# Optimization experiments

Measured on AMD Instinct MI355X. Metric: run time of the kernel, lower is better.

The kernel has to match this reference:

```python
import jax, jax.numpy as jnp
import numpy as np
from jax import lax

B, T, F = 64, 2048, 40
CF, K = 8, 3              # conv filters, kernel size
Ho, Wo = T - K + 1, F - K + 1   # valid conv output: (2046, 38)
GIN, GH, ATT = Wo * CF, 32, 32  # GRU input 304, hidden 32, attn 32


def setup_inputs() -> dict:
    key = jax.random.key(0)
    ks = jax.random.split(key, 16)
    s = 0.1
    return {
        "x": jax.random.normal(ks[0], (B, 1, T, F), jnp.float32),
        "offset_w": jax.random.normal(ks[1], (2 * K * K, 1, K, K), jnp.float32) * s,
        "offset_b": jnp.zeros((2 * K * K,), jnp.float32),
        "dcn_w": jax.random.normal(ks[2], (CF, 1, K, K), jnp.float32) * s,
        "dcn_b": jax.random.normal(ks[3], (CF,), jnp.float32) * s,
        "w_ih": jax.random.normal(ks[4], (3 * GH, GIN), jnp.float32) * s,
        "w_hh": jax.random.normal(ks[5], (3 * GH, GH), jnp.float32) * s,
        "b_ih": jax.random.normal(ks[6], (3 * GH,), jnp.float32) * s,
        "b_hh": jax.random.normal(ks[7], (3 * GH,), jnp.float32) * s,
        "w1": jax.random.normal(ks[8], (ATT, GH), jnp.float32) * s,
        "b1": jax.random.normal(ks[9], (ATT,), jnp.float32) * s,
        "w2": jax.random.normal(ks[10], (GH, ATT), jnp.float32) * s,
        "b2": jax.random.normal(ks[11], (GH,), jnp.float32) * s,
        "w3": jax.random.normal(ks[12], (2, GH), jnp.float32) * s,
        "b3": jax.random.normal(ks[13], (2,), jnp.float32) * s,
    }


def _bilinear(img, ph, pw):
    # img: (H, W); ph, pw: (Ho, Wo, K*K) float sampling coords
    H, W = img.shape
    ph = jnp.clip(ph, 0.0, H - 1.0)
    pw = jnp.clip(pw, 0.0, W - 1.0)
    h0 = jnp.floor(ph).astype(jnp.int32)
    w0 = jnp.floor(pw).astype(jnp.int32)
    h1 = jnp.minimum(h0 + 1, H - 1)
    w1 = jnp.minimum(w0 + 1, W - 1)
    lh = ph - h0.astype(ph.dtype)
    lw = pw - w0.astype(pw.dtype)
    v00 = img[h0, w0]
    v01 = img[h0, w1]
    v10 = img[h1, w0]
    v11 = img[h1, w1]
    return (v00 * (1 - lh) * (1 - lw) + v01 * (1 - lh) * lw
            + v10 * lh * (1 - lw) + v11 * lh * lw)


def _deform_conv(x, offset_w, offset_b, dcn_w, dcn_b):
    # offset conv (valid): (B, 2*K*K, Ho, Wo)
    offset = lax.conv_general_dilated(
        x, offset_w, (1, 1), 'VALID',
        dimension_numbers=('NCHW', 'OIHW', 'NCHW')) + offset_b[None, :, None, None]
    off_h = offset[:, :K * K].transpose(0, 2, 3, 1)   # (B, Ho, Wo, 9)
    off_w = offset[:, K * K:].transpose(0, 2, 3, 1)
    ki = jnp.repeat(jnp.arange(K, dtype=x.dtype), K)  # kernel row index per tap
    kj = jnp.tile(jnp.arange(K, dtype=x.dtype), K)    # kernel col index per tap
    base_h = (jnp.arange(Ho, dtype=x.dtype)[:, None] + ki)[:, None, :]  # (Ho,1,9)
    base_w = (jnp.arange(Wo, dtype=x.dtype)[:, None] + kj)[None, :, :]  # (1,Wo,9)
    ph = off_h + base_h   # (B, Ho, Wo, 9)
    pw = off_w + base_w
    samp = jax.vmap(_bilinear)(x[:, 0], ph, pw)       # (B, Ho, Wo, 9)
    out = jnp.einsum('bhwk,ok->bohw', samp, dcn_w.reshape(CF, K * K))
    out = out + dcn_b[None, :, None, None]            # (B, CF, Ho, Wo)
    return out, offset


def _gru(xs, w_ih, w_hh, b_ih, b_hh):
    # xs: (T, B, GIN); PyTorch GRU gate order r, z, n
    gi_all = jnp.einsum('tbi,gi->tbg', xs, w_ih) + b_ih  # precompute input gates
    h0 = jnp.zeros((xs.shape[1], GH), xs.dtype)

    def step(h, gi):
        gh = h @ w_hh.T + b_hh
        ir, iz, inn = jnp.split(gi, 3, axis=-1)
        hr, hz, hn = jnp.split(gh, 3, axis=-1)
        r = jax.nn.sigmoid(ir + hr)
        z = jax.nn.sigmoid(iz + hz)
        n = jnp.tanh(inn + r * hn)
        h = (1 - z) * n + z * h
        return h, h

    _, ys = lax.scan(step, h0, gi_all)
    return ys  # (T, B, GH)


def reference(x, offset_w, offset_b, dcn_w, dcn_b,
              w_ih, w_hh, b_ih, b_hh, w1, b1, w2, b2, w3, b3):
    out_dcn, offset = _deform_conv(x, offset_w, offset_b, dcn_w, dcn_b)
    # (B, CF, Ho, Wo) -> (Ho, B, Wo, CF) -> (Ho, B, Wo*CF)
    h = out_dcn.transpose(2, 0, 3, 1).reshape(Ho, B, GIN)
    out_gru = _gru(h, w_ih, w_hh, b_ih, b_hh)         # (Ho, B, GH)
    enc = out_gru.transpose(1, 0, 2)                   # (B, Ho, GH)
    a = jnp.tanh(enc @ w1.T + b1)                      # (B, Ho, ATT)
    out_l2 = a @ w2.T + b2                             # (B, Ho, GH)
    out_sm = jax.nn.softmax(out_l2, axis=1)            # softmax over time
    out_mul = out_sm * enc
    out_sum = out_mul.sum(axis=1)                      # (B, GH)
    logits = out_sum @ w3.T + b3                       # (B, 2)
    return (logits, out_sum, out_mul, out_sm, out_l2, out_gru, out_dcn, dcn_w, dcn_b)
```

## Files before the change

### kernel.cpp

```cpp
#include <hip/hip_runtime.h>
#include <math.h>

#define NB 64
#define NT 2048
#define NF 40
#define HO 2046
#define WO 38
#define HW 77748
#define GIN 304
#define NG 96
#define GH 32

#define OFF_LOGITS 0
#define OFF_SUM    128
#define OFF_MUL    2176
#define OFF_SM     4192384
#define OFF_L2     8382592
#define OFF_GRU    12572800
#define OFF_DCN    16763008
#define OFF_DCNW   56569984
#define OFF_DCNB   56570056
#define OFF_GI     OFF_MUL
#define OFF_WIHR   OFF_GRU

#define CG_SCALE (-1.44269504088896340736f)
#define CN_SCALE ( 2.88539008177792681472f)

typedef float f32x2 __attribute__((ext_vector_type(2)));
typedef float f32x4 __attribute__((ext_vector_type(4)));
typedef short bf16x8 __attribute__((ext_vector_type(8)));
typedef unsigned long long u64;

__device__ __forceinline__ float rcp_f(float x){
  return __builtin_amdgcn_rcpf(x);
}
__device__ __forceinline__ float sigmoid_f(float x){
  return rcp_f(1.0f + __expf(-x));
}
__device__ __forceinline__ float tanh_f(float x){
  return 1.0f - 2.0f * rcp_f(__expf(2.0f * x) + 1.0f);
}
__device__ __forceinline__ unsigned bf16r(float x){
  unsigned u = __float_as_uint(x);
  return (u + 0x7FFFu + ((u >> 16) & 1u)) >> 16;
}

#define WKP 328
__global__ void k0_prep(const float* __restrict__ w_ih, const float* __restrict__ dcn_w,
                        const float* __restrict__ dcn_b, float* __restrict__ dout)
{
  int i = blockIdx.x * 256 + threadIdx.x;
  unsigned short* wb = (unsigned short*)(dout + OFF_WIHR);
  if (i < NG * WKP){
    int g = i / WKP, kk = i - g * WKP;
    unsigned short v = 0;
    if (kk < GIN){
      int cf = kk / WO, wo = kk - cf * WO;
      v = (unsigned short)bf16r(w_ih[g * GIN + wo * 8 + cf]);
    }
    wb[i] = v;
  } else if (i < NG * WKP + 72){
    dout[OFF_DCNW + (i - NG * WKP)] = dcn_w[i - NG * WKP];
  } else if (i < NG * WKP + 80){
    dout[OFF_DCNB + (i - NG * WKP - 72)] = dcn_b[i - NG * WKP - 72];
  }
}

#define XLR 26
__global__ __launch_bounds__(256, 6) void k1_deform(
    const float* __restrict__ x, const float* __restrict__ offset_w,
    const float* __restrict__ offset_b, const float* __restrict__ dcn_w,
    const float* __restrict__ dcn_b, float* __restrict__ out_dcn)
{
  __shared__ f32x2 owp[81];
  __shared__ f32x2 obp[9];
  __shared__ f32x2 dwp[4][9];
  __shared__ float db[8];
  __shared__ float xl[XLR][41];
  int tid = threadIdx.x;
  if (tid < 81) owp[tid] = (f32x2){offset_w[tid], offset_w[81 + tid]};
  if (tid < 9)  obp[tid] = (f32x2){offset_b[tid], offset_b[9 + tid]};
  if (tid < 36){
    int q = tid / 9, tap = tid - q * 9;
    dwp[q][tap] = (f32x2){dcn_w[(2 * q) * 9 + tap], dcn_w[(2 * q + 1) * 9 + tap]};
  }
  if (tid < 8)  db[tid] = dcn_b[tid];

  int b = blockIdx.y;
  const float* xb = x + (size_t)b * NT * NF;
  int h_base = 2 * ((blockIdx.x * 256) / WO);
  for (int i = tid; i < XLR * NF; i += 256){
    int r = i / NF, cc = i - r * NF;
    int gr = h_base - 3 + r;
    gr = min(max(gr, 0), NT - 1);
    xl[r][cc] = xb[(size_t)gr * NF + cc];
  }
  __syncthreads();

  int idx = blockIdx.x * 256 + tid;
  if (idx >= 1023 * WO) return;
  int ho2 = idx / WO, wo = idx - ho2 * WO;
  int ho = ho2 * 2;
  int hrel = ho - h_base + 3;

  float patch[12];
  #pragma unroll
  for (int p = 0; p < 4; p++)
    #pragma unroll
    for (int q = 0; q < 3; q++)
      patch[p * 3 + q] = xl[hrel + p][wo + q];

  f32x2 acc0[4], acc1[4];
  #pragma unroll
  for (int q = 0; q < 4; q++){
    acc0[q] = (f32x2){db[2 * q], db[2 * q + 1]};
    acc1[q] = acc0[q];
  }

  #pragma unroll
  for (int tap = 0; tap < 9; tap++){
    f32x2 off0 = obp[tap], off1 = off0;
    #pragma unroll
    for (int t2 = 0; t2 < 9; t2++){
      f32x2 wp = owp[tap * 9 + t2];
      off0 += wp * (f32x2){patch[t2], patch[t2]};
      off1 += wp * (f32x2){patch[3 + t2], patch[3 + t2]};
    }
    int tr = tap / 3, tc = tap % 3;
    #pragma unroll
    for (int pt = 0; pt < 2; pt++){
      f32x2 off = pt ? off1 : off0;
      float ph = off.x + (float)(ho + pt + tr);
      float pw = off.y + (float)(wo + tc);
      ph = fminf(fmaxf(ph, 0.0f), (float)(NT - 1));
      pw = fminf(fmaxf(pw, 0.0f), (float)(NF - 1));
      int h0 = (int)floorf(ph);
      int w0 = (int)floorf(pw);
      int h1 = min(h0 + 1, NT - 1);
      int w1 = min(w0 + 1, NF - 1);
      float lh = ph - (float)h0;
      float lw = pw - (float)w0;
      int hi0 = h0 - h_base + 3;
      int hi1 = h1 - h_base + 3;
      float v00 = xl[hi0][w0], v01 = xl[hi0][w1];
      float v10 = xl[hi1][w0], v11 = xl[hi1][w1];
      float s = v00 * (1.0f - lh) * (1.0f - lw) + v01 * (1.0f - lh) * lw
              + v10 * lh * (1.0f - lw) + v11 * lh * lw;
      f32x2 sp = {s, s};
      f32x2* ac = pt ? acc1 : acc0;
      #pragma unroll
      for (int q = 0; q < 4; q++) ac[q] += dwp[q][tap] * sp;
    }
  }
  size_t base = (size_t)(b * 8) * HW + (size_t)ho * WO + wo;
  #pragma unroll
  for (int q = 0; q < 4; q++){
    out_dcn[base + (size_t)(2 * q) * HW]          = acc0[q].x;
    out_dcn[base + (size_t)(2 * q + 1) * HW]      = acc0[q].y;
    out_dcn[base + (size_t)(2 * q) * HW + WO]     = acc1[q].x;
    out_dcn[base + (size_t)(2 * q + 1) * HW + WO] = acc1[q].y;
  }
}

#define K2_M 128
__global__ __launch_bounds__(512) void k2_gi(
    const float* __restrict__ dro,
    const float* __restrict__ b_ih, const float* __restrict__ b_hh,
    float* __restrict__ gi)
{
  __shared__ unsigned short xsl[K2_M][WKP];
  __shared__ unsigned short wl[NG][WKP];
  int tid = threadIdx.x;
  int tile = blockIdx.x;
  int b = blockIdx.y;
  int t0 = tile * K2_M;
  const float* dcn = dro + OFF_DCN;
  const uint4* wbf = (const uint4*)(dro + OFF_WIHR);

  {
    uint4* dst = (uint4*)&wl[0][0];
    for (int i = tid; i < NG * WKP / 8; i += 512) dst[i] = wbf[i];
  }
  for (int i = tid; i < K2_M * 152; i += 512){
    int tt = i / 152, p = i - tt * 152;
    int t = t0 + tt;
    int kp = 2 * p; int cf = kp / WO; int wo = kp - cf * WO;
    unsigned v = 0;
    if (t < HO){
      float2 xv = *(const float2*)&dcn[((size_t)(b * 8 + cf) * HO + t) * WO + wo];
      v = bf16r(xv.x) | (bf16r(xv.y) << 16);
    }
    *(unsigned*)&xsl[tt][kp] = v;
  }
  for (int i = tid; i < K2_M * 12; i += 512){
    int tt = i / 12, p = i - tt * 12;
    *(unsigned*)&xsl[tt][GIN + 2 * p] = 0;
  }
  __syncthreads();

  int wv = tid >> 6, l = tid & 63;
  int r16 = l & 15, koct = l >> 4;
  f32x4 acc[6];
  #pragma unroll
  for (int n = 0; n < 6; n++) acc[n] = (f32x4){0.0f, 0.0f, 0.0f, 0.0f};

  #pragma unroll
  for (int ks = 0; ks < 10; ks++){
    int kb = ks * 32 + koct * 8;
    bf16x8 af = *(const bf16x8*)&xsl[wv * 16 + r16][kb];
    #pragma unroll
    for (int n = 0; n < 6; n++){
      bf16x8 bfr = *(const bf16x8*)&wl[n * 16 + r16][kb];
      acc[n] = __builtin_amdgcn_mfma_f32_16x16x32_bf16(af, bfr, acc[n], 0, 0, 0);
    }
  }
  #pragma unroll
  for (int n = 0; n < 6; n++){
    int g = n * 16 + r16;
    float sc = (g < 64) ? CG_SCALE : CN_SCALE;
    float bb = b_ih[g] + ((g < 64) ? b_hh[g] : 0.0f);
    #pragma unroll
    for (int reg = 0; reg < 4; reg++){
      int t = t0 + wv * 16 + koct * 4 + reg;
      if (t < HO)
        gi[((size_t)b * HO + t) * NG + g] = (acc[n][reg] + bb) * sc;
    }
  }
}

#define CHUNKS 32
#define CLEN 64
#define BURN 64
__global__ __launch_bounds__(64) __attribute__((amdgpu_waves_per_eu(1, 2)))
void k3_gru(
    const float* __restrict__ gi, const float* __restrict__ w_hh,
    const float* __restrict__ b_hh, float* __restrict__ out_gru)
{
  int b = blockIdx.x;
  int c = blockIdx.y;
  int lane = threadIdx.x;
  int j = lane & 31;
  f32x2 wgp[16], wnp[16];
  #pragma unroll
  for (int m = 0; m < 16; m++){
    wgp[m].x = w_hh[lane * GH + 2 * m]     * CG_SCALE;
    wgp[m].y = w_hh[lane * GH + 2 * m + 1] * CG_SCALE;
    wnp[m].x = w_hh[(64 + j) * GH + 2 * m]     * CN_SCALE;
    wnp[m].y = w_hh[(64 + j) * GH + 2 * m + 1] * CN_SCALE;
  }
  float bn = b_hh[64 + j] * CN_SCALE;
  #pragma unroll
  for (int m = 0; m < 16; m++){
    asm volatile("" : "+v"(wgp[m]), "+v"(wnp[m]));
  }
  asm volatile("" : "+v"(bn));

  __shared__ __align__(16) float hl[64];

  int sstart = c * CLEN;
  int t0 = (c == 0) ? 0 : (sstart - BURN);
  int tend = min(sstart + CLEN, HO);
  int nsteps = tend - t0;
  int nblk = (nsteps + 7) >> 3;

  const float* gip = gi + ((size_t)b * HO + t0) * NG;
  float* og = out_gru + (size_t)b * GH + j;

  float Ag[8], An[8], Bg[8], Bn[8];
  float hj = 0.0f;

  #define LOADBLK(G_, N_, BLK_)                                              \
  {                                                                          \
    const float* p_ = gip + (size_t)(BLK_) * (8 * NG);                       \
    _Pragma("unroll")                                                        \
    for (int s = 0; s < 8; s++){                                             \
      G_[s] = p_[s * NG + lane];         \
      N_[s] = p_[s * NG + 64 + j];                     \
    }                                                                        \
  }

  #define QUAD(Q_, MA_)                                                      \
  {                                                                          \
    f32x2 pA_ = {Q_.x, Q_.y};                                                \
    f32x2 pB_ = {Q_.z, Q_.w};                                                \
    asm("v_pk_fma_f32 %0, %1, %2, %0" : "+v"(ag0) : "v"(wgp[MA_]),     "v"(pA_)); \
    asm("v_pk_fma_f32 %0, %1, %2, %0" : "+v"(an0) : "v"(wnp[MA_]),     "v"(pA_)); \
    asm("v_pk_fma_f32 %0, %1, %2, %0" : "+v"(ag1) : "v"(wgp[MA_ + 1]), "v"(pB_)); \
    asm("v_pk_fma_f32 %0, %1, %2, %0" : "+v"(an1) : "v"(wnp[MA_ + 1]), "v"(pB_)); \
  }

  #define GRU_STEP(GG_, GN_, HS_)                                            \
  {                                                                          \
    hl[lane] = hj;                            \
    asm volatile("" ::: "memory");          \
    f32x4 q0 = *(const f32x4*)&hl[0];                                        \
    f32x4 q1 = *(const f32x4*)&hl[4];                                        \
    f32x4 q2 = *(const f32x4*)&hl[8];                                        \
    f32x4 q3 = *(const f32x4*)&hl[12];                                       \
    f32x4 q4 = *(const f32x4*)&hl[16];                                       \
    f32x4 q5 = *(const f32x4*)&hl[20];                                       \
    f32x4 q6 = *(const f32x4*)&hl[24];                                       \
    f32x4 q7 = *(const f32x4*)&hl[28];                                       \
    f32x2 ag0 = {0.0f, 0.0f}, ag1 = {0.0f, 0.0f};                            \
    f32x2 an0 = {0.0f, 0.0f}, an1 = {0.0f, 0.0f};                            \
    QUAD(q0, 0)  QUAD(q1, 2)  QUAD(q2, 4)  QUAD(q3, 6)                       \
    QUAD(q4, 8)  QUAD(q5, 10) QUAD(q6, 12) QUAD(q7, 14)                      \
    float sg = (ag0.x + ag0.y) + (ag1.x + ag1.y);                            \
    float sn = (an0.x + an0.y) + (an1.x + an1.y) + bn;                       \
    float g  = rcp_f(1.0f + __builtin_amdgcn_exp2f(GG_ + sg));               \
    float zc = __shfl_xor(g, 32, 64);                  \
    float nv = fmaf(-2.0f,                                                   \
        rcp_f(__builtin_amdgcn_exp2f(fmaf(g, sn, GN_)) + 1.0f), 1.0f);       \
    hj = fmaf(zc, hj - nv, nv);                     \
    HS_ = hj;                                                                \
  }

  #define COMPUTE8(G_, N_, BLKI_)                                            \
  {                                                                          \
    float hsv[8];                                                            \
    _Pragma("unroll")                                                        \
    for (int s = 0; s < 8; s++){ GRU_STEP(G_[s], N_[s], hsv[s]); }           \
    int tb_ = t0 + (BLKI_) * 8;                                              \
    if (lane < 32){                                                          \
      _Pragma("unroll")                                                      \
      for (int s = 0; s < 8; s++){                                           \
        int t_ = tb_ + s;                                                    \
        if (t_ >= sstart && t_ < tend)                                       \
          og[(size_t)t_ * (NB * GH)] = hsv[s];                               \
      }                                                                      \
    }                                                                        \
  }

  LOADBLK(Ag, An, 0);
  LOADBLK(Bg, Bn, 1);
  int npair = nblk >> 1;
  for (int p = 0; p < npair; p++){
    int i0 = 2 * p;
    COMPUTE8(Ag, An, i0);
    if (i0 + 2 < nblk) LOADBLK(Ag, An, i0 + 2);
    COMPUTE8(Bg, Bn, i0 + 1);
    if (i0 + 3 < nblk) LOADBLK(Bg, Bn, i0 + 3);
  }
  #undef LOADBLK
  #undef QUAD
  #undef GRU_STEP
  #undef COMPUTE8
}

__global__ __launch_bounds__(256) void k4a_att(
    const float* __restrict__ out_gru,
    const float* __restrict__ w1, const float* __restrict__ b1,
    const float* __restrict__ w2, const float* __restrict__ b2,
    float* __restrict__ out_l2)
{
  __shared__ float w1p[32][33], w2p[32][33], encl[64][32], al[64][33];
  __shared__ float b1l[32], b2l[32];
  int tid = threadIdx.x;
  int tile = blockIdx.x;
  int b = blockIdx.y;
  if (tid < 32){ b1l[tid] = b1[tid]; b2l[tid] = b2[tid]; }
  for (int i = tid; i < 1024; i += 256){
    int jj = i >> 5, kk = i & 31;
    w1p[jj][kk] = w1[i];
    w2p[jj][kk] = w2[i];
  }
  int t0 = tile * 64;
  for (int i = tid; i < 64 * 32; i += 256){
    int tt = i >> 5, kk = i & 31;
    int t = t0 + tt;
    encl[tt][kk] = (t < HO) ? out_gru[((size_t)t * NB + b) * GH + kk] : 0.0f;
  }
  __syncthreads();
  int j = tid & 31, tq = tid >> 5;
  #pragma unroll
  for (int pass = 0; pass < 8; pass++){
    int tt = pass * 8 + tq;
    float a = b1l[j];
    #pragma unroll
    for (int k = 0; k < 32; k++) a += encl[tt][k] * w1p[j][k];
    al[tt][j] = tanh_f(a);
  }
  __syncthreads();
  #pragma unroll
  for (int pass = 0; pass < 8; pass++){
    int tt = pass * 8 + tq;
    float v = b2l[j];
    #pragma unroll
    for (int k = 0; k < 32; k++) v += al[tt][k] * w2p[j][k];
    int t = t0 + tt;
    if (t < HO) out_l2[((size_t)b * HO + t) * GH + j] = v;
  }
}

__global__ __launch_bounds__(1024) void k4b_soft(
    const float* __restrict__ out_l2, const float* __restrict__ out_gru,
    const float* __restrict__ w3, const float* __restrict__ b3,
    float* __restrict__ dout)
{
  __shared__ float ml[32][32], sl[32][32];
  __shared__ float Mf[32], rSf[32];
  __shared__ float pl[32][32];
  __shared__ float osum[32];
  int tid = threadIdx.x;
  int b = blockIdx.x;
  int j = tid & 31, tg = tid >> 5;
  const float* l2b = out_l2 + (size_t)b * HO * GH;
  float m = -INFINITY, s = 0.0f;
  for (int t = tg; t < HO; t += 32){
    float v = l2b[t * GH + j];
    float mn = fmaxf(m, v);
    s = s * __expf(m - mn) + __expf(v - mn);
    m = mn;
  }
  ml[tg][j] = m; sl[tg][j] = s;
  __syncthreads();
  if (tid < 32){
    float M = -INFINITY;
    #pragma unroll
    for (int i = 0; i < 32; i++) M = fmaxf(M, ml[i][tid]);
    float S = 0.0f;
    #pragma unroll
    for (int i = 0; i < 32; i++) S += sl[i][tid] * __expf(ml[i][tid] - M);
    Mf[tid] = M; rSf[tid] = 1.0f / S;
  }
  __syncthreads();
  float M = Mf[j], rS = rSf[j];
  float ps = 0.0f;
  float* sm_o  = dout + OFF_SM  + (size_t)b * HO * GH;
  float* mul_o = dout + OFF_MUL + (size_t)b * HO * GH;
  for (int t = tg; t < HO; t += 32){
    float v = l2b[t * GH + j];
    float e = __expf(v - M) * rS;
    float enc = out_gru[((size_t)t * NB + b) * GH + j];
    sm_o[t * GH + j] = e;
    float mu = e * enc;
    mul_o[t * GH + j] = mu;
    ps += mu;
  }
  pl[tg][j] = ps;
  __syncthreads();
  if (tid < 32){
    float S2 = 0.0f;
    #pragma unroll
    for (int i = 0; i < 32; i++) S2 += pl[i][tid];
    dout[OFF_SUM + b * GH + tid] = S2;
    osum[tid] = S2;
  }
  __syncthreads();
  if (tid < 2){
    float L = b3[tid];
    #pragma unroll
    for (int k = 0; k < 32; k++) L += w3[tid * GH + k] * osum[k];
    dout[OFF_LOGITS + b * 2 + tid] = L;
  }
}

extern "C" void kernel_launch(void* const* d_in, const int* in_sizes, int n_in,
                              void* d_out, int out_size, void* d_ws, size_t ws_size,
                              hipStream_t stream)
{
  const float* x        = (const float*)d_in[0];
  const float* offset_w = (const float*)d_in[1];
  const float* offset_b = (const float*)d_in[2];
  const float* dcn_w    = (const float*)d_in[3];
  const float* dcn_b    = (const float*)d_in[4];
  const float* w_ih     = (const float*)d_in[5];
  const float* w_hh     = (const float*)d_in[6];
  const float* b_ih     = (const float*)d_in[7];
  const float* b_hh     = (const float*)d_in[8];
  const float* w1       = (const float*)d_in[9];
  const float* b1       = (const float*)d_in[10];
  const float* w2       = (const float*)d_in[11];
  const float* b2       = (const float*)d_in[12];
  const float* w3       = (const float*)d_in[13];
  const float* b3       = (const float*)d_in[14];
  float* dout = (float*)d_out;
  (void)in_sizes; (void)n_in; (void)out_size; (void)d_ws; (void)ws_size;

  k0_prep<<<124, 256, 0, stream>>>(w_ih, dcn_w, dcn_b, dout);
  k1_deform<<<dim3(152, NB), 256, 0, stream>>>(x, offset_w, offset_b, dcn_w, dcn_b,
                                               dout + OFF_DCN);
  k2_gi<<<dim3(16, NB), 512, 0, stream>>>(dout, b_ih, b_hh, dout + OFF_GI);
  k3_gru<<<dim3(NB, CHUNKS), 64, 0, stream>>>(dout + OFF_GI, w_hh, b_hh,
                                              dout + OFF_GRU);
  k4a_att<<<dim3(32, NB), 256, 0, stream>>>(dout + OFF_GRU, w1, b1, w2, b2,
                                            dout + OFF_L2);
  k4b_soft<<<NB, 1024, 0, stream>>>(dout + OFF_L2, dout + OFF_GRU, w3, b3, dout);
}
```

Before: 285.5 us.

## Split softmax-over-time into chunked partial max/sum, normalize, and finalize kernels

Replaces the single 64-block softmax/attention-sum kernel with three kernels: per-chunk online max/sum over 4 time chunks, a normalize pass that writes softmax and weighted outputs plus partial sums, and a small finalize kernel for the sum and logits. The aim is to spread the work over 256 blocks instead of 64, which should fill more of the GPU's compute units. In exchange it adds two extra kernel launches and a workspace round trip. It falls back to the old kernel if the workspace is too small.

```diff
diff --git a/kernel.cpp b/kernel.cpp
--- a/kernel.cpp
+++ b/kernel.cpp
@@ -392,6 +392,102 @@
   }
 }
 
+#define K4Q 512
+__global__ __launch_bounds__(256) void k4b1_ms(
+    const float* __restrict__ out_l2, float* __restrict__ ws)
+{
+  __shared__ float ml[8][32], sl[8][32];
+  int q = blockIdx.x, b = blockIdx.y;
+  int tid = threadIdx.x;
+  int j = tid & 31, tg = tid >> 5;
+  const float* l2b = out_l2 + (size_t)b * HO * GH;
+  int t1 = min((q + 1) * K4Q, HO);
+  float m = -INFINITY, s = 0.0f;
+  for (int t = q * K4Q + tg; t < t1; t += 8){
+    float v = l2b[t * GH + j];
+    float mn = fmaxf(m, v);
+    s = s * __expf(m - mn) + __expf(v - mn);
+    m = mn;
+  }
+  ml[tg][j] = m; sl[tg][j] = s;
+  __syncthreads();
+  if (tid < 32){
+    float M = -INFINITY;
+    #pragma unroll
+    for (int i = 0; i < 8; i++) M = fmaxf(M, ml[i][tid]);
+    float S = 0.0f;
+    #pragma unroll
+    for (int i = 0; i < 8; i++) S += sl[i][tid] * __expf(ml[i][tid] - M);
+    ws[((size_t)(b * 4 + q) * 32 + tid) * 2]     = M;
+    ws[((size_t)(b * 4 + q) * 32 + tid) * 2 + 1] = S;
+  }
+}
+
+__global__ __launch_bounds__(256) void k4b2_norm(
+    const float* __restrict__ out_l2, const float* __restrict__ out_gru,
+    float* __restrict__ ws, float* __restrict__ dout)
+{
+  __shared__ float pl[8][32];
+  int q = blockIdx.x, b = blockIdx.y;
+  int tid = threadIdx.x;
+  int j = tid & 31, tg = tid >> 5;
+  float M = -INFINITY;
+  #pragma unroll
+  for (int i = 0; i < 4; i++)
+    M = fmaxf(M, ws[((size_t)(b * 4 + i) * 32 + j) * 2]);
+  float S = 0.0f;
+  #pragma unroll
+  for (int i = 0; i < 4; i++){
+    float mq = ws[((size_t)(b * 4 + i) * 32 + j) * 2];
+    float sq = ws[((size_t)(b * 4 + i) * 32 + j) * 2 + 1];
+    S += sq * __expf(mq - M);
+  }
+  float rS = 1.0f / S;
+  const float* l2b = out_l2 + (size_t)b * HO * GH;
+  float* sm_o  = dout + OFF_SM  + (size_t)b * HO * GH;
+  float* mul_o = dout + OFF_MUL + (size_t)b * HO * GH;
+  int t1 = min((q + 1) * K4Q, HO);
+  float ps = 0.0f;
+  for (int t = q * K4Q + tg; t < t1; t += 8){
+    float v = l2b[t * GH + j];
+    float e = __expf(v - M) * rS;
+    float enc = out_gru[((size_t)t * NB + b) * GH + j];
+    sm_o[t * GH + j] = e;
+    float mu = e * enc;
+    mul_o[t * GH + j] = mu;
+    ps += mu;
+  }
+  pl[tg][j] = ps;
+  __syncthreads();
+  if (tid < 32){
+    float P = 0.0f;
+    #pragma unroll
+    for (int i = 0; i < 8; i++) P += pl[i][tid];
+    ws[16384 + (size_t)(b * 4 + q) * 32 + tid] = P;
+  }
+}
+
+__global__ __launch_bounds__(32) void k4b3_fin(
+    const float* __restrict__ ws, const float* __restrict__ w3,
+    const float* __restrict__ b3, float* __restrict__ dout)
+{
+  __shared__ float osum[32];
+  int b = blockIdx.x;
+  int j = threadIdx.x;
+  float S2 = 0.0f;
+  #pragma unroll
+  for (int i = 0; i < 4; i++) S2 += ws[16384 + (size_t)(b * 4 + i) * 32 + j];
+  dout[OFF_SUM + b * GH + j] = S2;
+  osum[j] = S2;
+  __syncthreads();
+  if (j < 2){
+    float L = b3[j];
+    #pragma unroll
+    for (int k = 0; k < 32; k++) L += w3[j * GH + k] * osum[k];
+    dout[OFF_LOGITS + b * 2 + j] = L;
+  }
+}
+
 __global__ __launch_bounds__(1024) void k4b_soft(
     const float* __restrict__ out_l2, const float* __restrict__ out_gru,
     const float* __restrict__ w3, const float* __restrict__ b3,
@@ -475,7 +571,8 @@
   const float* w3       = (const float*)d_in[13];
   const float* b3       = (const float*)d_in[14];
   float* dout = (float*)d_out;
-  (void)in_sizes; (void)n_in; (void)out_size; (void)d_ws; (void)ws_size;
+  float* ws   = (float*)d_ws;
+  (void)in_sizes; (void)n_in; (void)out_size;
 
   k0_prep<<<124, 256, 0, stream>>>(w_ih, dcn_w, dcn_b, dout);
   k1_deform<<<dim3(152, NB), 256, 0, stream>>>(x, offset_w, offset_b, dcn_w, dcn_b,
@@ -485,5 +582,12 @@
                                               dout + OFF_GRU);
   k4a_att<<<dim3(32, NB), 256, 0, stream>>>(dout + OFF_GRU, w1, b1, w2, b2,
                                             dout + OFF_L2);
-  k4b_soft<<<NB, 1024, 0, stream>>>(dout + OFF_L2, dout + OFF_GRU, w3, b3, dout);
-}
+  if (ws_size >= (16384 + 8192) * sizeof(float)){
+    k4b1_ms<<<dim3(4, NB), 256, 0, stream>>>(dout + OFF_L2, ws);
+    k4b2_norm<<<dim3(4, NB), 256, 0, stream>>>(dout + OFF_L2, dout + OFF_GRU,
+                                               ws, dout);
+    k4b3_fin<<<NB, 32, 0, stream>>>(ws, w3, b3, dout);
+  } else {
+    k4b_soft<<<NB, 1024, 0, stream>>>(dout + OFF_L2, dout + OFF_GRU, w3, b3, dout);
+  }
+}
```

Result: no change. 285.2 us (-0.1%).
